# Optimization experiments

Measured on AMD Instinct MI355X. Metric: run time of the kernel, lower is better.

The kernel has to match this reference:

```python
import jax, jax.numpy as jnp
import numpy as np
import math

D_MODEL = 768
B, S = 8, 2048


def setup_inputs() -> dict:
    key = jax.random.key(0)
    k1, k2, k3, k4, k5 = jax.random.split(key, 5)
    return {
        "input": jax.random.normal(k1, (B, S, D_MODEL), dtype=jnp.float32),
        "attention_mask": jax.random.randint(k2, (B,), 0, S + 1, dtype=jnp.int32),
        "Wq": jax.random.normal(k3, (D_MODEL, D_MODEL), dtype=jnp.float32),
        "Wk": jax.random.normal(k4, (D_MODEL, D_MODEL), dtype=jnp.float32),
        "Wv": jax.random.normal(k5, (D_MODEL, D_MODEL), dtype=jnp.float32),
    }


def reference(input, attention_mask, Wq, Wk, Wv):
    d_model = Wq.shape[0]
    # QKV projections (v is computed in the original but never used in the output)
    q = jnp.matmul(input, Wq)  # [B,S,D]
    k = jnp.matmul(input, Wk)  # [B,S,D]
    v = jnp.matmul(input, Wv)  # [B,S,D] (dead in original forward output)
    # Per-sample QK^T, vectorized instead of the original python loop+cat
    attention_score = jnp.einsum("bqd,bkd->bqk", q, k) / math.sqrt(float(d_model) ** 3)
    # Ragged mask: positions (j,k) with j<len_i and k<len_i keep the score, else -1000.
    # Built with vectorized arange comparisons instead of the original triple python loop.
    idx = jnp.arange(attention_score.shape[1])  # [S]
    valid = idx[None, :] < attention_mask[:, None]  # [B,S]
    keep = valid[:, :, None] & valid[:, None, :]  # [B,S,S]
    mask_attention_score = jnp.where(keep, attention_score, jnp.float32(-1000.0))
    attention_score_n = jax.nn.softmax(mask_attention_score, axis=-1)  # computed but unused, as in original
    # Original returns UNMASKED, pre-softmax scores matmul'd with the raw input (not v).
    self_attention = jnp.einsum("bqk,bkd->bqd", attention_score, input)
    return self_attention
```

## Files before the change

kernel.cpp:

```cpp
#include <hip/hip_runtime.h>
#include <cmath>


typedef __attribute__((ext_vector_type(8))) short short8;
typedef __attribute__((ext_vector_type(4))) float f32x4;

__device__ __forceinline__ unsigned short f2bf(float f) {
    union { float f; unsigned int u; } v; v.f = f;
    unsigned int u = v.u;
    return (unsigned short)((u + 0x7FFFu + ((u >> 16) & 1u)) >> 16);
}

template <int NIT>
__device__ __forceinline__ void setup_stage(const unsigned short* base, int ld, int tid,
                                            const unsigned short* (&gp)[NIT])
{
    #pragma unroll
    for (int it = 0; it < NIT; ++it) {
        int slot = it * 256 + tid, r = slot >> 3, c = slot & 7;
        gp[it] = base + (size_t)r * ld + ((c ^ (r & 7)) << 3);
    }
}

template <int NIT>
__device__ __forceinline__ void stage_adv(const unsigned short* const (&gp)[NIT], int koff,
                                          unsigned short* ldsbase, int tid)
{
    #pragma unroll
    for (int it = 0; it < NIT; ++it) {
        unsigned short* lp = ldsbase + (size_t)(it * 256 + (tid & 192)) * 8;
        __builtin_amdgcn_global_load_lds(
            (__attribute__((address_space(1))) void*)(void*)(gp[it] + koff),
            (__attribute__((address_space(3))) void*)lp, 16, 0, 0);
    }
}

template <int F>
__device__ __forceinline__ void frag_offs(int wbase, int l15, int quad, int (&o)[F][2])
{
    #pragma unroll
    for (int i = 0; i < F; ++i) {
        int r = wbase + i * 16 + l15;
        o[i][0] = r * 64 + ((quad ^ (r & 7)) << 3);
        o[i][1] = r * 64 + (((quad + 4) ^ (r & 7)) << 3);
    }
}

template <int FM, int FN>
__device__ __forceinline__ void mfma_frags(const unsigned short* __restrict__ Al,
                                           const unsigned short* __restrict__ Bl,
                                           const int (&oA)[FM][2], const int (&oB)[FN][2],
                                           f32x4 (&acc)[FM][FN])
{
    short8 af[FM][2], bfr[FN][2];
    #pragma unroll
    for (int i = 0; i < FM; ++i) {
        af[i][0] = *reinterpret_cast<const short8*>(&Al[oA[i][0]]);
        af[i][1] = *reinterpret_cast<const short8*>(&Al[oA[i][1]]);
    }
    #pragma unroll
    for (int i = 0; i < FN; ++i) {
        bfr[i][0] = *reinterpret_cast<const short8*>(&Bl[oB[i][0]]);
        bfr[i][1] = *reinterpret_cast<const short8*>(&Bl[oB[i][1]]);
    }
    #pragma unroll
    for (int ks = 0; ks < 2; ++ks)
        #pragma unroll
        for (int mi = 0; mi < FM; ++mi)
            #pragma unroll
            for (int ni = 0; ni < FN; ++ni)
                acc[mi][ni] = __builtin_amdgcn_mfma_f32_16x16x32_bf16(
                    af[mi][ks], bfr[ni][ks], acc[mi][ni], 0, 0, 0);
}

template <int ROWS>
__device__ __forceinline__ void stage_f32(const float* __restrict__ src, unsigned short* lds,
                                          int ld, int tid)
{
    #pragma unroll
    for (int it = 0; it < ROWS / 32; ++it) {
        int slot = it * 256 + tid;
        int r = slot >> 3, c = slot & 7;
        const float* gp = src + (size_t)r * ld + c * 8;
        float4 a = *reinterpret_cast<const float4*>(gp);
        float4 d = *reinterpret_cast<const float4*>(gp + 4);
        union { short8 s; unsigned short u[8]; } v;
        v.u[0] = f2bf(a.x); v.u[1] = f2bf(a.y); v.u[2] = f2bf(a.z); v.u[3] = f2bf(a.w);
        v.u[4] = f2bf(d.x); v.u[5] = f2bf(d.y); v.u[6] = f2bf(d.z); v.u[7] = f2bf(d.w);
        *reinterpret_cast<short8*>(&lds[r * 64 + ((c ^ (r & 7)) << 3)]) = v.s;
    }
}

__device__ __forceinline__ void store_c(float* C, size_t i, float v) { C[i] = v; }
__device__ __forceinline__ void store_c(unsigned short* C, size_t i, float v) { C[i] = f2bf(v); }

template <int TM, int TN, typename CT>
__device__ __forceinline__ void epilogue(CT* __restrict__ C, f32x4 (&acc)[TM / 32][TN / 32],
                                         int rowBase, int colBase, int ldc, float alpha,
                                         int wr, int wc, int l15, int quad)
{
    #pragma unroll
    for (int mi = 0; mi < TM / 32; ++mi)
        #pragma unroll
        for (int ni = 0; ni < TN / 32; ++ni) {
            int col = colBase + wc + ni * 16 + l15;
            #pragma unroll
            for (int r = 0; r < 4; ++r) {
                int row = rowBase + wr + mi * 16 + quad * 4 + r;
                store_c(C, (size_t)row * ldc + col, alpha * acc[mi][ni][r]);
            }
        }
}

__global__ __launch_bounds__(256)
void prep(const float* __restrict__ X, const float* __restrict__ Wq,
          const float* __restrict__ Wk, unsigned short* __restrict__ Xt,
          unsigned short* __restrict__ Xbf, unsigned short* __restrict__ P16)
{
    __shared__ unsigned short lds[(64 + 64) * 64];
    const int blk = blockIdx.x;
    const int tid = threadIdx.x, lane = tid & 63, wave = tid >> 6;
    const int l15 = lane & 15, quad = lane >> 4;

    if (blk < 144) {
        const int ty = blk / 12, tz = blk - ty * 12;
        const int wr = (wave >> 1) * 32, wc = (wave & 1) * 32;
        int oA[2][2], oB[2][2];
        frag_offs<2>(wr, l15, quad, oA);
        frag_offs<2>(wc, l15, quad, oB);
        f32x4 acc[2][2] = {};
        for (int k0 = 0; k0 < 768; k0 += 64) {
            stage_f32<64>(Wq + (size_t)ty * 64 * 768 + k0, lds, 768, tid);
            stage_f32<64>(Wk + (size_t)tz * 64 * 768 + k0, lds + 64 * 64, 768, tid);
            __syncthreads();
            mfma_frags<2, 2>(lds, lds + 64 * 64, oA, oB, acc);
            __syncthreads();
        }
        epilogue<64, 64, unsigned short>(P16, acc, ty * 64, tz * 64, 768, 1.0f,
                                         wr, wc, l15, quad);
        return;
    }

    const int t0 = blk - 144;
    const int b = t0 & 7;
    const int tile = t0 >> 3;
    const int s0 = (tile & 31) * 64;
    const int d0 = (tile >> 5) * 64;
    const float* Xb = X + (size_t)b * 2048 * 768;
    unsigned short* Xtb = Xt + (size_t)b * 2048 * 768;
    unsigned short* Xbb = Xbf + (size_t)b * 2048 * 768;
    unsigned short* T = lds;

    const int mr = threadIdx.x >> 4;
    const int mc = threadIdx.x & 15;

    const float* src = &Xb[(size_t)(s0 + 4 * mr) * 768 + d0 + 4 * mc];
    float4 v0 = *reinterpret_cast<const float4*>(src);
    float4 v1 = *reinterpret_cast<const float4*>(src + 768);
    float4 v2 = *reinterpret_cast<const float4*>(src + 2 * 768);
    float4 v3 = *reinterpret_cast<const float4*>(src + 3 * 768);
    ushort4 r0 = { f2bf(v0.x), f2bf(v0.y), f2bf(v0.z), f2bf(v0.w) };
    ushort4 r1 = { f2bf(v1.x), f2bf(v1.y), f2bf(v1.z), f2bf(v1.w) };
    ushort4 r2 = { f2bf(v2.x), f2bf(v2.y), f2bf(v2.z), f2bf(v2.w) };
    ushort4 r3 = { f2bf(v3.x), f2bf(v3.y), f2bf(v3.z), f2bf(v3.w) };
    unsigned short* dstb = &Xbb[(size_t)(s0 + 4 * mr) * 768 + d0 + 4 * mc];
    *reinterpret_cast<ushort4*>(dstb)            = r0;
    *reinterpret_cast<ushort4*>(dstb + 768)      = r1;
    *reinterpret_cast<ushort4*>(dstb + 2 * 768)  = r2;
    *reinterpret_cast<ushort4*>(dstb + 3 * 768)  = r3;

    ushort4 c0 = { r0.x, r1.x, r2.x, r3.x };
    ushort4 c1 = { r0.y, r1.y, r2.y, r3.y };
    ushort4 c2 = { r0.z, r1.z, r2.z, r3.z };
    ushort4 c3 = { r0.w, r1.w, r2.w, r3.w };
    {
        int d;
        d = 4 * mc + 0; *reinterpret_cast<ushort4*>(&T[d * 64 + ((mr ^ (2 * (d & 7))) & 15) * 4]) = c0;
        d = 4 * mc + 1; *reinterpret_cast<ushort4*>(&T[d * 64 + ((mr ^ (2 * (d & 7))) & 15) * 4]) = c1;
        d = 4 * mc + 2; *reinterpret_cast<ushort4*>(&T[d * 64 + ((mr ^ (2 * (d & 7))) & 15) * 4]) = c2;
        d = 4 * mc + 3; *reinterpret_cast<ushort4*>(&T[d * 64 + ((mr ^ (2 * (d & 7))) & 15) * 4]) = c3;
    }
    __syncthreads();
    #pragma unroll
    for (int p = 0; p < 2; ++p) {
        int d  = p * 32 + (threadIdx.x >> 3);
        int q0 = 2 * (threadIdx.x & 7);
        int c  = (q0 ^ (2 * (d & 7))) & 15;
        short8 o = *reinterpret_cast<const short8*>(&T[d * 64 + c * 4]);
        *reinterpret_cast<short8*>(&Xtb[(size_t)(d0 + d) * 2048 + s0 + q0 * 4]) = o;
    }
}

__global__ __launch_bounds__(256)
void gemm_G(const unsigned short* __restrict__ Xt, float* __restrict__ Ga,
            float* __restrict__ Gb)
{
    __shared__ unsigned short lds[2][(96 + 96) * 64];
    const int blk = blockIdx.x;
    const int b  = blk & 7;
    const int ks = (blk >> 3) & 1;
    const int u  = blk >> 4;
    int ty = 0, rem = u, len = 8;
    while (rem >= len) { rem -= len; --len; ++ty; }
    const int tz = ty + rem;
    const bool diag = (ty == tz);

    const int tid = threadIdx.x, lane = tid & 63, wave = tid >> 6;
    const int wr = (wave >> 1) * 48, wc = (wave & 1) * 48;
    const int l15 = lane & 15, quad = lane >> 4;

    const unsigned short* Xtb = Xt + (size_t)b * 768 * 2048;
    const unsigned short* A0 = Xtb + (size_t)ty * 96 * 2048 + ks * 1024;
    const unsigned short* B0 = Xtb + (size_t)tz * 96 * 2048 + ks * 1024;
    float* C = (ks ? Gb : Ga) + (size_t)b * 768 * 768;

    const unsigned short* gA[3]; const unsigned short* gB[3];
    setup_stage<3>(A0, 2048, tid, gA);
    setup_stage<3>(B0, 2048, tid, gB);
    int oA[3][2], oB[3][2];
    frag_offs<3>(wr, l15, quad, oA);
    frag_offs<3>(wc, l15, quad, oB);
    const int bbase = diag ? 0 : 96 * 64;

    f32x4 acc[3][3] = {};
    stage_adv<3>(gA, 0, &lds[0][0], tid);
    if (!diag) stage_adv<3>(gB, 0, &lds[0][96 * 64], tid);
    __syncthreads();

    const int nt = 16;
    for (int t = 0; t < nt; ++t) {
        const int cur = t & 1;
        if (t + 1 < nt) {
            stage_adv<3>(gA, (t + 1) * 64, &lds[cur ^ 1][0], tid);
            if (!diag) stage_adv<3>(gB, (t + 1) * 64, &lds[cur ^ 1][96 * 64], tid);
        }
        mfma_frags<3, 3>(&lds[cur][0], &lds[cur][bbase], oA, oB, acc);
        __syncthreads();
    }

    #pragma unroll
    for (int mi = 0; mi < 3; ++mi)
        #pragma unroll
        for (int ni = 0; ni < 3; ++ni) {
            int col = tz * 96 + wc + ni * 16 + l15;
            int row0 = ty * 96 + wr + mi * 16 + quad * 4;
            #pragma unroll
            for (int r = 0; r < 4; ++r)
                C[(size_t)(row0 + r) * 768 + col] = acc[mi][ni][r];
            if (!diag) {
                float4 m = { acc[mi][ni][0], acc[mi][ni][1],
                             acc[mi][ni][2], acc[mi][ni][3] };
                *reinterpret_cast<float4*>(&C[(size_t)col * 768 + row0]) = m;
            }
        }
}

__global__ __launch_bounds__(256)
void gemm_Ht(const float* __restrict__ Ga, const float* __restrict__ Gb,
             const unsigned short* __restrict__ P16, unsigned short* __restrict__ Ht,
             float alpha)
{
    __shared__ unsigned short lds[2][(96 + 96) * 64];
    const int b = blockIdx.x, ty = blockIdx.y, tz = blockIdx.z;
    const int tid = threadIdx.x, lane = tid & 63, wave = tid >> 6;
    const int wr = (wave >> 1) * 48, wc = (wave & 1) * 48;
    const int l15 = lane & 15, quad = lane >> 4;

    const float* Ab = Ga + (size_t)b * 768 * 768 + (size_t)ty * 96 * 768;
    const float* Bb = Gb + (size_t)b * 768 * 768 + (size_t)ty * 96 * 768;
    const unsigned short* B0 = P16 + (size_t)tz * 96 * 768;

    size_t pOff[3]; int pLds[3];
    #pragma unroll
    for (int it = 0; it < 3; ++it) {
        int slot = it * 256 + tid, r = slot >> 3, c = slot & 7;
        pOff[it] = (size_t)r * 768 + c * 8;
        pLds[it] = r * 64 + ((c ^ (r & 7)) << 3);
    }
    const unsigned short* gB[3];
    setup_stage<3>(B0, 768, tid, gB);
    int oA[3][2], oB[3][2];
    frag_offs<3>(wr, l15, quad, oA);
    frag_offs<3>(wc, l15, quad, oB);

    auto pair_stage = [&](int koff, unsigned short* dst) {
        #pragma unroll
        for (int it = 0; it < 3; ++it) {
            size_t off = pOff[it] + koff;
            float4 a0 = *reinterpret_cast<const float4*>(Ab + off);
            float4 a1 = *reinterpret_cast<const float4*>(Ab + off + 4);
            float4 b0 = *reinterpret_cast<const float4*>(Bb + off);
            float4 b1 = *reinterpret_cast<const float4*>(Bb + off + 4);
            union { short8 s; unsigned short u[8]; } v;
            v.u[0] = f2bf(a0.x + b0.x); v.u[1] = f2bf(a0.y + b0.y);
            v.u[2] = f2bf(a0.z + b0.z); v.u[3] = f2bf(a0.w + b0.w);
            v.u[4] = f2bf(a1.x + b1.x); v.u[5] = f2bf(a1.y + b1.y);
            v.u[6] = f2bf(a1.z + b1.z); v.u[7] = f2bf(a1.w + b1.w);
            *reinterpret_cast<short8*>(&dst[pLds[it]]) = v.s;
        }
    };

    f32x4 acc[3][3] = {};
    pair_stage(0, &lds[0][0]);
    stage_adv<3>(gB, 0, &lds[0][96 * 64], tid);
    __syncthreads();

    const int nt = 12;
    for (int t = 0; t < nt; ++t) {
        const int cur = t & 1;
        if (t + 1 < nt) {
            stage_adv<3>(gB, (t + 1) * 64, &lds[cur ^ 1][96 * 64], tid);
            pair_stage((t + 1) * 64, &lds[cur ^ 1][0]);
        }
        mfma_frags<3, 3>(&lds[cur][0], &lds[cur][96 * 64], oA, oB, acc);
        __syncthreads();
    }
    epilogue<96, 96, unsigned short>(Ht + (size_t)b * 768 * 768, acc,
                                     ty * 96, tz * 96, 768, alpha, wr, wc, l15, quad);
}

__global__ __launch_bounds__(256)
void gemm_out(const unsigned short* __restrict__ Xbf, const unsigned short* __restrict__ Ht,
              float* __restrict__ out)
{
    __shared__ unsigned short lds[2][(128 + 128) * 64];
    const int b = blockIdx.x, ty = blockIdx.y, tz = blockIdx.z;
    const int tid = threadIdx.x, lane = tid & 63, wave = tid >> 6;
    const int wr = (wave >> 1) * 64, wc = (wave & 1) * 64;
    const int l15 = lane & 15, quad = lane >> 4;

    const unsigned short* A0 = Xbf + (size_t)b * 2048 * 768 + (size_t)ty * 128 * 768;
    const unsigned short* B0 = Ht + (size_t)b * 768 * 768 + (size_t)tz * 128 * 768;

    const unsigned short* gA[4]; const unsigned short* gB[4];
    setup_stage<4>(A0, 768, tid, gA);
    setup_stage<4>(B0, 768, tid, gB);
    int oA[4][2], oB[4][2];
    frag_offs<4>(wr, l15, quad, oA);
    frag_offs<4>(wc, l15, quad, oB);

    f32x4 acc[4][4] = {};
    stage_adv<4>(gA, 0, &lds[0][0], tid);
    stage_adv<4>(gB, 0, &lds[0][128 * 64], tid);
    __syncthreads();

    const int nt = 12;
    for (int t = 0; t < nt; ++t) {
        const int cur = t & 1;
        if (t + 1 < nt) {
            stage_adv<4>(gA, (t + 1) * 64, &lds[cur ^ 1][0], tid);
            stage_adv<4>(gB, (t + 1) * 64, &lds[cur ^ 1][128 * 64], tid);
        }
        mfma_frags<4, 4>(&lds[cur][0], &lds[cur][128 * 64], oA, oB, acc);
        __syncthreads();
    }
    epilogue<128, 128, float>(out + (size_t)b * 2048 * 768, acc,
                              ty * 128, tz * 128, 768, 1.0f, wr, wc, l15, quad);
}

extern "C" void kernel_launch(void* const* d_in, const int* in_sizes, int n_in,
                              void* d_out, int out_size, void* d_ws, size_t ws_size,
                              hipStream_t stream)
{
    const float* X  = (const float*)d_in[0];
    const float* Wq = (const float*)d_in[2];
    const float* Wk = (const float*)d_in[3];
    float* out = (float*)d_out;

    const int Bn = 8, S = 2048, D = 768;
    const float alpha = 1.0f / (768.0f * sqrtf(768.0f));
    const size_t szX  = (size_t)Bn * S * D;
    const size_t szDD = (size_t)Bn * D * D;

    unsigned short* Xt  = (unsigned short*)d_ws;
    unsigned short* Xbf = Xt + szX;
    unsigned short* P16 = Xbf + szX;
    float* Ga = (float*)(P16 + (size_t)D * D);
    float* Gb = Ga + szDD;
    unsigned short* Ht = (unsigned short*)(Gb + szDD);

    prep<<<dim3(144 + Bn * (S / 64) * (D / 64)), 256, 0, stream>>>(X, Wq, Wk, Xt, Xbf, P16);

    gemm_G<<<dim3(576), 256, 0, stream>>>(Xt, Ga, Gb);

    gemm_Ht<<<dim3(Bn, 8, 8), 256, 0, stream>>>(Ga, Gb, P16, Ht, alpha);

    gemm_out<<<dim3(Bn, S / 128, 6), 256, 0, stream>>>(Xbf, Ht, out);
}
```

Baseline: 184.0 us.

## Triple-buffer LDS pipelines in gemm_G and gemm_out; narrow gemm_out N tile

Both gemm_G and gemm_out move from a double-buffered LDS loop to a three-stage ring. Each iteration waits on vmcnt and a raw s_barrier instead of a full __syncthreads, which keeps two tiles of global loads in flight. gemm_out's output tile shrinks from 128x128 to 128x64 and its grid doubles, aiming for more blocks and better occupancy under the larger LDS footprint. gemm_G drops its diagonal special case and now always loads the B tile, which adds redundant loads for diagonal blocks. The hand-tuned vmcnt counts depend on how many loads stage_adv issues, and a wrong count would break correctness.

```diff
diff --git a/kernel.cpp b/kernel.cpp
--- a/kernel.cpp
+++ b/kernel.cpp
@@ -195,7 +195,8 @@
 void gemm_G(const unsigned short* __restrict__ Xt, float* __restrict__ Ga,
             float* __restrict__ Gb)
 {
-    __shared__ unsigned short lds[2][(96 + 96) * 64];
+    constexpr int BUF = (96 + 96) * 64;
+    __shared__ unsigned short lds[3 * BUF];
     const int blk = blockIdx.x;
     const int b  = blk & 7;
     const int ks = (blk >> 3) & 1;
@@ -203,7 +204,6 @@
     int ty = 0, rem = u, len = 8;
     while (rem >= len) { rem -= len; --len; ++ty; }
     const int tz = ty + rem;
-    const bool diag = (ty == tz);
 
     const int tid = threadIdx.x, lane = tid & 63, wave = tid >> 6;
     const int wr = (wave >> 1) * 48, wc = (wave & 1) * 48;
@@ -220,22 +220,29 @@
     int oA[3][2], oB[3][2];
     frag_offs<3>(wr, l15, quad, oA);
     frag_offs<3>(wc, l15, quad, oB);
-    const int bbase = diag ? 0 : 96 * 64;
+
+    unsigned short* q0 = lds;
+    unsigned short* q1 = lds + BUF;
+    unsigned short* q2 = lds + 2 * BUF;
 
     f32x4 acc[3][3] = {};
-    stage_adv<3>(gA, 0, &lds[0][0], tid);
-    if (!diag) stage_adv<3>(gB, 0, &lds[0][96 * 64], tid);
-    __syncthreads();
+    stage_adv<3>(gA, 0, q0, tid);
+    stage_adv<3>(gB, 0, q0 + 96 * 64, tid);
+    stage_adv<3>(gA, 64, q1, tid);
+    stage_adv<3>(gB, 64, q1 + 96 * 64, tid);
 
     const int nt = 16;
     for (int t = 0; t < nt; ++t) {
-        const int cur = t & 1;
-        if (t + 1 < nt) {
-            stage_adv<3>(gA, (t + 1) * 64, &lds[cur ^ 1][0], tid);
-            if (!diag) stage_adv<3>(gB, (t + 1) * 64, &lds[cur ^ 1][96 * 64], tid);
-        }
-        mfma_frags<3, 3>(&lds[cur][0], &lds[cur][bbase], oA, oB, acc);
-        __syncthreads();
+        if (t < nt - 1) asm volatile("s_waitcnt vmcnt(6)" ::: "memory");
+        else            asm volatile("s_waitcnt vmcnt(0)" ::: "memory");
+        __builtin_amdgcn_s_barrier();
+        __builtin_amdgcn_sched_barrier(0);
+        if (t + 2 < nt) {
+            stage_adv<3>(gA, (t + 2) * 64, q2, tid);
+            stage_adv<3>(gB, (t + 2) * 64, q2 + 96 * 64, tid);
+        }
+        mfma_frags<3, 3>(q0, q0 + 96 * 64, oA, oB, acc);
+        unsigned short* tmp = q0; q0 = q1; q1 = q2; q2 = tmp;
     }
 
     #pragma unroll
@@ -247,7 +254,7 @@
             #pragma unroll
             for (int r = 0; r < 4; ++r)
                 C[(size_t)(row0 + r) * 768 + col] = acc[mi][ni][r];
-            if (!diag) {
+            if (ty != tz) {
                 float4 m = { acc[mi][ni][0], acc[mi][ni][1],
                              acc[mi][ni][2], acc[mi][ni][3] };
                 *reinterpret_cast<float4*>(&C[(size_t)col * 768 + row0]) = m;
@@ -323,39 +330,48 @@
 void gemm_out(const unsigned short* __restrict__ Xbf, const unsigned short* __restrict__ Ht,
               float* __restrict__ out)
 {
-    __shared__ unsigned short lds[2][(128 + 128) * 64];
+    constexpr int BUF = (128 + 64) * 64;
+    __shared__ unsigned short lds[3 * BUF];
     const int b = blockIdx.x, ty = blockIdx.y, tz = blockIdx.z;
     const int tid = threadIdx.x, lane = tid & 63, wave = tid >> 6;
-    const int wr = (wave >> 1) * 64, wc = (wave & 1) * 64;
+    const int wr = (wave >> 1) * 64, wc = (wave & 1) * 32;
     const int l15 = lane & 15, quad = lane >> 4;
 
     const unsigned short* A0 = Xbf + (size_t)b * 2048 * 768 + (size_t)ty * 128 * 768;
-    const unsigned short* B0 = Ht + (size_t)b * 768 * 768 + (size_t)tz * 128 * 768;
-
-    const unsigned short* gA[4]; const unsigned short* gB[4];
+    const unsigned short* B0 = Ht + (size_t)b * 768 * 768 + (size_t)tz * 64 * 768;
+
+    const unsigned short* gA[4]; const unsigned short* gB[2];
     setup_stage<4>(A0, 768, tid, gA);
-    setup_stage<4>(B0, 768, tid, gB);
-    int oA[4][2], oB[4][2];
+    setup_stage<2>(B0, 768, tid, gB);
+    int oA[4][2], oB[2][2];
     frag_offs<4>(wr, l15, quad, oA);
-    frag_offs<4>(wc, l15, quad, oB);
-
-    f32x4 acc[4][4] = {};
-    stage_adv<4>(gA, 0, &lds[0][0], tid);
-    stage_adv<4>(gB, 0, &lds[0][128 * 64], tid);
-    __syncthreads();
+    frag_offs<2>(wc, l15, quad, oB);
+
+    unsigned short* q0 = lds;
+    unsigned short* q1 = lds + BUF;
+    unsigned short* q2 = lds + 2 * BUF;
+
+    f32x4 acc[4][2] = {};
+    stage_adv<4>(gA, 0, q0, tid);
+    stage_adv<2>(gB, 0, q0 + 128 * 64, tid);
+    stage_adv<4>(gA, 64, q1, tid);
+    stage_adv<2>(gB, 64, q1 + 128 * 64, tid);
 
     const int nt = 12;
     for (int t = 0; t < nt; ++t) {
-        const int cur = t & 1;
-        if (t + 1 < nt) {
-            stage_adv<4>(gA, (t + 1) * 64, &lds[cur ^ 1][0], tid);
-            stage_adv<4>(gB, (t + 1) * 64, &lds[cur ^ 1][128 * 64], tid);
-        }
-        mfma_frags<4, 4>(&lds[cur][0], &lds[cur][128 * 64], oA, oB, acc);
-        __syncthreads();
-    }
-    epilogue<128, 128, float>(out + (size_t)b * 2048 * 768, acc,
-                              ty * 128, tz * 128, 768, 1.0f, wr, wc, l15, quad);
+        if (t < nt - 1) asm volatile("s_waitcnt vmcnt(6)" ::: "memory");
+        else            asm volatile("s_waitcnt vmcnt(0)" ::: "memory");
+        __builtin_amdgcn_s_barrier();
+        __builtin_amdgcn_sched_barrier(0);
+        if (t + 2 < nt) {
+            stage_adv<4>(gA, (t + 2) * 64, q2, tid);
+            stage_adv<2>(gB, (t + 2) * 64, q2 + 128 * 64, tid);
+        }
+        mfma_frags<4, 2>(q0, q0 + 128 * 64, oA, oB, acc);
+        unsigned short* tmp = q0; q0 = q1; q1 = q2; q2 = tmp;
+    }
+    epilogue<128, 64, float>(out + (size_t)b * 2048 * 768, acc,
+                             ty * 128, tz * 64, 768, 1.0f, wr, wc, l15, quad);
 }
 
 extern "C" void kernel_launch(void* const* d_in, const int* in_sizes, int n_in,
@@ -385,5 +401,5 @@
 
     gemm_Ht<<<dim3(Bn, 8, 8), 256, 0, stream>>>(Ga, Gb, P16, Ht, alpha);
 
-    gemm_out<<<dim3(Bn, S / 128, 6), 256, 0, stream>>>(Xbf, Ht, out);
-}
+    gemm_out<<<dim3(Bn, S / 128, 12), 256, 0, stream>>>(Xbf, Ht, out);
+}
```

After: 194.2 us. 1.06x slower.

## Compute Gram matrix without split-K in bf16 and move Wq·Wk^T into Gram kernel

Applied to the files above, without the earlier changes.

The Gram kernel X^T X now uses 64x64 tiles over the full K=2048 with no split-K, so it writes a single bf16 G16 instead of two fp32 partial buffers. This removes the fp32 partial-sum writes and the add-and-convert step in gemm_Ht, which can now use plain bf16 staging. The Wq·Wk^T product moves from prep into extra blocks of the Gram kernel. In exchange each Gram block runs a longer K loop on smaller tiles, and G is rounded to bf16 before the next GEMM, which may cost accuracy.

```diff
diff --git a/kernel.cpp b/kernel.cpp
--- a/kernel.cpp
+++ b/kernel.cpp
@@ -113,43 +113,18 @@
 }
 
 __global__ __launch_bounds__(256)
-void prep(const float* __restrict__ X, const float* __restrict__ Wq,
-          const float* __restrict__ Wk, unsigned short* __restrict__ Xt,
-          unsigned short* __restrict__ Xbf, unsigned short* __restrict__ P16)
-{
-    __shared__ unsigned short lds[(64 + 64) * 64];
+void prep(const float* __restrict__ X, unsigned short* __restrict__ Xt,
+          unsigned short* __restrict__ Xbf)
+{
+    __shared__ unsigned short T[64 * 64];
     const int blk = blockIdx.x;
-    const int tid = threadIdx.x, lane = tid & 63, wave = tid >> 6;
-    const int l15 = lane & 15, quad = lane >> 4;
-
-    if (blk < 144) {
-        const int ty = blk / 12, tz = blk - ty * 12;
-        const int wr = (wave >> 1) * 32, wc = (wave & 1) * 32;
-        int oA[2][2], oB[2][2];
-        frag_offs<2>(wr, l15, quad, oA);
-        frag_offs<2>(wc, l15, quad, oB);
-        f32x4 acc[2][2] = {};
-        for (int k0 = 0; k0 < 768; k0 += 64) {
-            stage_f32<64>(Wq + (size_t)ty * 64 * 768 + k0, lds, 768, tid);
-            stage_f32<64>(Wk + (size_t)tz * 64 * 768 + k0, lds + 64 * 64, 768, tid);
-            __syncthreads();
-            mfma_frags<2, 2>(lds, lds + 64 * 64, oA, oB, acc);
-            __syncthreads();
-        }
-        epilogue<64, 64, unsigned short>(P16, acc, ty * 64, tz * 64, 768, 1.0f,
-                                         wr, wc, l15, quad);
-        return;
-    }
-
-    const int t0 = blk - 144;
-    const int b = t0 & 7;
-    const int tile = t0 >> 3;
+    const int b = blk & 7;
+    const int tile = blk >> 3;
     const int s0 = (tile & 31) * 64;
     const int d0 = (tile >> 5) * 64;
     const float* Xb = X + (size_t)b * 2048 * 768;
     unsigned short* Xtb = Xt + (size_t)b * 2048 * 768;
     unsigned short* Xbb = Xbf + (size_t)b * 2048 * 768;
-    unsigned short* T = lds;
 
     const int mr = threadIdx.x >> 4;
     const int mc = threadIdx.x & 15;
@@ -192,73 +167,93 @@
 }
 
 __global__ __launch_bounds__(256)
-void gemm_G(const unsigned short* __restrict__ Xt, float* __restrict__ Ga,
-            float* __restrict__ Gb)
-{
-    __shared__ unsigned short lds[2][(96 + 96) * 64];
+void gemm_GP(const unsigned short* __restrict__ Xt, unsigned short* __restrict__ G16,
+             const float* __restrict__ Wq, const float* __restrict__ Wk,
+             unsigned short* __restrict__ P16)
+{
+    __shared__ unsigned short lds[2][(64 + 64) * 64];
     const int blk = blockIdx.x;
-    const int b  = blk & 7;
-    const int ks = (blk >> 3) & 1;
-    const int u  = blk >> 4;
-    int ty = 0, rem = u, len = 8;
-    while (rem >= len) { rem -= len; --len; ++ty; }
-    const int tz = ty + rem;
-    const bool diag = (ty == tz);
-
     const int tid = threadIdx.x, lane = tid & 63, wave = tid >> 6;
-    const int wr = (wave >> 1) * 48, wc = (wave & 1) * 48;
     const int l15 = lane & 15, quad = lane >> 4;
-
-    const unsigned short* Xtb = Xt + (size_t)b * 768 * 2048;
-    const unsigned short* A0 = Xtb + (size_t)ty * 96 * 2048 + ks * 1024;
-    const unsigned short* B0 = Xtb + (size_t)tz * 96 * 2048 + ks * 1024;
-    float* C = (ks ? Gb : Ga) + (size_t)b * 768 * 768;
-
-    const unsigned short* gA[3]; const unsigned short* gB[3];
-    setup_stage<3>(A0, 2048, tid, gA);
-    setup_stage<3>(B0, 2048, tid, gB);
-    int oA[3][2], oB[3][2];
-    frag_offs<3>(wr, l15, quad, oA);
-    frag_offs<3>(wc, l15, quad, oB);
-    const int bbase = diag ? 0 : 96 * 64;
-
-    f32x4 acc[3][3] = {};
-    stage_adv<3>(gA, 0, &lds[0][0], tid);
-    if (!diag) stage_adv<3>(gB, 0, &lds[0][96 * 64], tid);
-    __syncthreads();
-
-    const int nt = 16;
-    for (int t = 0; t < nt; ++t) {
-        const int cur = t & 1;
-        if (t + 1 < nt) {
-            stage_adv<3>(gA, (t + 1) * 64, &lds[cur ^ 1][0], tid);
-            if (!diag) stage_adv<3>(gB, (t + 1) * 64, &lds[cur ^ 1][96 * 64], tid);
-        }
-        mfma_frags<3, 3>(&lds[cur][0], &lds[cur][bbase], oA, oB, acc);
+    const int wr = (wave >> 1) * 32, wc = (wave & 1) * 32;
+
+    if (blk < 624) {
+        const int b = blk & 7;
+        const int u = blk >> 3;
+        int ty = 0, rem = u, len = 12;
+        while (rem >= len) { rem -= len; --len; ++ty; }
+        const int tz = ty + rem;
+        const bool diag = (ty == tz);
+
+        const unsigned short* Xtb = Xt + (size_t)b * 768 * 2048;
+        const unsigned short* A0 = Xtb + (size_t)ty * 64 * 2048;
+        const unsigned short* B0 = Xtb + (size_t)tz * 64 * 2048;
+        unsigned short* C = G16 + (size_t)b * 768 * 768;
+
+        const unsigned short* gA[2]; const unsigned short* gB[2];
+        setup_stage<2>(A0, 2048, tid, gA);
+        setup_stage<2>(B0, 2048, tid, gB);
+        int oA[2][2], oB[2][2];
+        frag_offs<2>(wr, l15, quad, oA);
+        frag_offs<2>(wc, l15, quad, oB);
+        const int bbase = diag ? 0 : 64 * 64;
+
+        f32x4 acc[2][2] = {};
+        stage_adv<2>(gA, 0, &lds[0][0], tid);
+        if (!diag) stage_adv<2>(gB, 0, &lds[0][64 * 64], tid);
         __syncthreads();
-    }
-
-    #pragma unroll
-    for (int mi = 0; mi < 3; ++mi)
+
+        const int nt = 32;
+        for (int t = 0; t < nt; ++t) {
+            const int cur = t & 1;
+            if (t + 1 < nt) {
+                stage_adv<2>(gA, (t + 1) * 64, &lds[cur ^ 1][0], tid);
+                if (!diag) stage_adv<2>(gB, (t + 1) * 64, &lds[cur ^ 1][64 * 64], tid);
+            }
+            mfma_frags<2, 2>(&lds[cur][0], &lds[cur][bbase], oA, oB, acc);
+            __syncthreads();
+        }
+
         #pragma unroll
-        for (int ni = 0; ni < 3; ++ni) {
-            int col = tz * 96 + wc + ni * 16 + l15;
-            int row0 = ty * 96 + wr + mi * 16 + quad * 4;
+        for (int mi = 0; mi < 2; ++mi)
             #pragma unroll
-            for (int r = 0; r < 4; ++r)
-                C[(size_t)(row0 + r) * 768 + col] = acc[mi][ni][r];
-            if (!diag) {
-                float4 m = { acc[mi][ni][0], acc[mi][ni][1],
-                             acc[mi][ni][2], acc[mi][ni][3] };
-                *reinterpret_cast<float4*>(&C[(size_t)col * 768 + row0]) = m;
+            for (int ni = 0; ni < 2; ++ni) {
+                int col = tz * 64 + wc + ni * 16 + l15;
+                int row0 = ty * 64 + wr + mi * 16 + quad * 4;
+                ushort4 m;
+                m.x = f2bf(acc[mi][ni][0]);
+                m.y = f2bf(acc[mi][ni][1]);
+                m.z = f2bf(acc[mi][ni][2]);
+                m.w = f2bf(acc[mi][ni][3]);
+                C[(size_t)(row0 + 0) * 768 + col] = m.x;
+                C[(size_t)(row0 + 1) * 768 + col] = m.y;
+                C[(size_t)(row0 + 2) * 768 + col] = m.z;
+                C[(size_t)(row0 + 3) * 768 + col] = m.w;
+                if (!diag)
+                    *reinterpret_cast<ushort4*>(&C[(size_t)col * 768 + row0]) = m;
             }
-        }
+    } else {
+        const int pb = blk - 624;
+        const int ty = pb / 12, tz = pb - ty * 12;
+        int oA[2][2], oB[2][2];
+        frag_offs<2>(wr, l15, quad, oA);
+        frag_offs<2>(wc, l15, quad, oB);
+        f32x4 acc[2][2] = {};
+        for (int k0 = 0; k0 < 768; k0 += 64) {
+            stage_f32<64>(Wq + (size_t)ty * 64 * 768 + k0, &lds[0][0], 768, tid);
+            stage_f32<64>(Wk + (size_t)tz * 64 * 768 + k0, &lds[0][64 * 64], 768, tid);
+            __syncthreads();
+            mfma_frags<2, 2>(&lds[0][0], &lds[0][64 * 64], oA, oB, acc);
+            __syncthreads();
+        }
+        epilogue<64, 64, unsigned short>(P16, acc, ty * 64, tz * 64, 768, 1.0f,
+                                         wr, wc, l15, quad);
+    }
 }
 
 __global__ __launch_bounds__(256)
-void gemm_Ht(const float* __restrict__ Ga, const float* __restrict__ Gb,
-             const unsigned short* __restrict__ P16, unsigned short* __restrict__ Ht,
-             float alpha)
+void gemm_Ht(const unsigned short* __restrict__ G16, const unsigned short* __restrict__ P16,
+             unsigned short* __restrict__ Ht, float alpha)
 {
     __shared__ unsigned short lds[2][(96 + 96) * 64];
     const int b = blockIdx.x, ty = blockIdx.y, tz = blockIdx.z;
@@ -266,42 +261,18 @@
     const int wr = (wave >> 1) * 48, wc = (wave & 1) * 48;
     const int l15 = lane & 15, quad = lane >> 4;
 
-    const float* Ab = Ga + (size_t)b * 768 * 768 + (size_t)ty * 96 * 768;
-    const float* Bb = Gb + (size_t)b * 768 * 768 + (size_t)ty * 96 * 768;
+    const unsigned short* A0 = G16 + (size_t)b * 768 * 768 + (size_t)ty * 96 * 768;
     const unsigned short* B0 = P16 + (size_t)tz * 96 * 768;
 
-    size_t pOff[3]; int pLds[3];
-    #pragma unroll
-    for (int it = 0; it < 3; ++it) {
-        int slot = it * 256 + tid, r = slot >> 3, c = slot & 7;
-        pOff[it] = (size_t)r * 768 + c * 8;
-        pLds[it] = r * 64 + ((c ^ (r & 7)) << 3);
-    }
-    const unsigned short* gB[3];
+    const unsigned short* gA[3]; const unsigned short* gB[3];
+    setup_stage<3>(A0, 768, tid, gA);
     setup_stage<3>(B0, 768, tid, gB);
     int oA[3][2], oB[3][2];
     frag_offs<3>(wr, l15, quad, oA);
     frag_offs<3>(wc, l15, quad, oB);
 
-    auto pair_stage = [&](int koff, unsigned short* dst) {
-        #pragma unroll
-        for (int it = 0; it < 3; ++it) {
-            size_t off = pOff[it] + koff;
-            float4 a0 = *reinterpret_cast<const float4*>(Ab + off);
-            float4 a1 = *reinterpret_cast<const float4*>(Ab + off + 4);
-            float4 b0 = *reinterpret_cast<const float4*>(Bb + off);
-            float4 b1 = *reinterpret_cast<const float4*>(Bb + off + 4);
-            union { short8 s; unsigned short u[8]; } v;
-            v.u[0] = f2bf(a0.x + b0.x); v.u[1] = f2bf(a0.y + b0.y);
-            v.u[2] = f2bf(a0.z + b0.z); v.u[3] = f2bf(a0.w + b0.w);
-            v.u[4] = f2bf(a1.x + b1.x); v.u[5] = f2bf(a1.y + b1.y);
-            v.u[6] = f2bf(a1.z + b1.z); v.u[7] = f2bf(a1.w + b1.w);
-            *reinterpret_cast<short8*>(&dst[pLds[it]]) = v.s;
-        }
-    };
-
     f32x4 acc[3][3] = {};
-    pair_stage(0, &lds[0][0]);
+    stage_adv<3>(gA, 0, &lds[0][0], tid);
     stage_adv<3>(gB, 0, &lds[0][96 * 64], tid);
     __syncthreads();
 
@@ -309,8 +280,8 @@
     for (int t = 0; t < nt; ++t) {
         const int cur = t & 1;
         if (t + 1 < nt) {
+            stage_adv<3>(gA, (t + 1) * 64, &lds[cur ^ 1][0], tid);
             stage_adv<3>(gB, (t + 1) * 64, &lds[cur ^ 1][96 * 64], tid);
-            pair_stage((t + 1) * 64, &lds[cur ^ 1][0]);
         }
         mfma_frags<3, 3>(&lds[cur][0], &lds[cur][96 * 64], oA, oB, acc);
         __syncthreads();
@@ -375,15 +346,14 @@
     unsigned short* Xt  = (unsigned short*)d_ws;
     unsigned short* Xbf = Xt + szX;
     unsigned short* P16 = Xbf + szX;
-    float* Ga = (float*)(P16 + (size_t)D * D);
-    float* Gb = Ga + szDD;
-    unsigned short* Ht = (unsigned short*)(Gb + szDD);
-
-    prep<<<dim3(144 + Bn * (S / 64) * (D / 64)), 256, 0, stream>>>(X, Wq, Wk, Xt, Xbf, P16);
-
-    gemm_G<<<dim3(576), 256, 0, stream>>>(Xt, Ga, Gb);
-
-    gemm_Ht<<<dim3(Bn, 8, 8), 256, 0, stream>>>(Ga, Gb, P16, Ht, alpha);
+    unsigned short* G16 = P16 + (size_t)D * D;
+    unsigned short* Ht  = G16 + szDD;
+
+    prep<<<dim3(Bn * (S / 64) * (D / 64)), 256, 0, stream>>>(X, Xt, Xbf);
+
+    gemm_GP<<<dim3(768), 256, 0, stream>>>(Xt, G16, Wq, Wk, P16);
+
+    gemm_Ht<<<dim3(Bn, 8, 8), 256, 0, stream>>>(G16, P16, Ht, alpha);
 
     gemm_out<<<dim3(Bn, S / 128, 6), 256, 0, stream>>>(Xbf, Ht, out);
 }
```

After: 180.6 us. Within noise of the previous version (-1.8%).
